# Kernel optimization log

Hardware: AMD Instinct MI355X
Metric: run time of the kernel (lower is better)

The kernel has to match this reference:

```python
import jax, jax.numpy as jnp
import numpy as np

E = 8        # num_experts
TOPK = 2     # num_experts_per_tok
D = 1024     # n_embd
H = 2816     # grok FFN hidden dim (multiple_of-rounded 2/3*4*D)
B, T = 4, 2048
COEFF = 0.01 # moe_aux_loss_coeff


def setup_inputs() -> dict:
    key = jax.random.key(0)
    ks = jax.random.split(key, 8)
    s = 0.02  # weight scale so activations stay well-conditioned
    return {
        "x": jax.random.normal(ks[0], (B, T, D), jnp.float32),
        "gate_w": jax.random.normal(ks[1], (D, E), jnp.float32) * s,
        "expert_gate": jax.random.normal(ks[2], (E, D, H), jnp.float32) * s,
        "expert_up": jax.random.normal(ks[3], (E, D, H), jnp.float32) * s,
        "expert_down": jax.random.normal(ks[4], (E, H, D), jnp.float32) * s,
        "shared_gate": jax.random.normal(ks[5], (D, H), jnp.float32) * s,
        "shared_up": jax.random.normal(ks[6], (D, H), jnp.float32) * s,
        "shared_down": jax.random.normal(ks[7], (H, D), jnp.float32) * s,
    }


def _grok_ffn(x, g, u, d):
    # down(gelu(gate(x)) * up(x)); torch F.gelu default = exact erf gelu
    return (jax.nn.gelu(x @ g, approximate=False) * (x @ u)) @ d


def reference(x, gate_w, expert_gate, expert_up, expert_down,
              shared_gate, shared_up, shared_down):
    Bb, Tt, Dd = x.shape
    N = Bb * Tt
    xf = x.reshape(N, Dd)

    # --- router ---
    logits = (xf @ gate_w).astype(jnp.float32)            # (N, E)
    top_logits, top_idx = jax.lax.top_k(logits, TOPK)     # (N, K)
    top_w = jax.nn.softmax(top_logits, axis=-1)           # (N, K)
    gates = jax.nn.softmax(logits, axis=-1)               # (N, E)
    f = jnp.mean(jax.nn.one_hot(top_idx[:, 0], E, dtype=jnp.float32), axis=0)
    P = gates.mean(axis=0)
    aux_loss = COEFF * E * jnp.sum(f * P)

    # dense combine weights (N, E): 0 for unassigned experts
    comb = jnp.zeros((N, E), xf.dtype).at[
        jnp.arange(N)[:, None], top_idx].add(top_w.astype(xf.dtype))

    # --- experts: loop over small fixed E, weight-masked dense FFN ---
    out = jnp.zeros_like(xf)
    for e in range(E):
        ye = _grok_ffn(xf, expert_gate[e], expert_up[e], expert_down[e])
        out = out + comb[:, e:e + 1] * ye

    out = out.reshape(Bb, Tt, Dd)
    out = out + _grok_ffn(xf, shared_gate, shared_up, shared_down).reshape(Bb, Tt, Dd)
    return out, aux_loss
```

## Files before the change

kernel.cpp:

```cpp
#include <hip/hip_runtime.h>
#include <hip/hip_bf16.h>

#define NTOK 8192
#define DIM  1024
#define HID  2816
#define ROWS_CAP 25600
#define TCAP 200

typedef __bf16 bf16x8 __attribute__((ext_vector_type(8)));
typedef float  f32x4  __attribute__((ext_vector_type(4)));

__device__ __forceinline__ unsigned short f2bf(float f) {
  unsigned int x = __float_as_uint(f);
  unsigned int r = (x + 0x7fffu + ((x >> 16) & 1u)) >> 16;
  return (unsigned short)r;
}
__device__ __forceinline__ float gelu_erf(float g) {
  return 0.5f * g * (1.0f + erff(g * 0.70710678118654752f));
}

__device__ __forceinline__ void gload16(const void* g, void* l) {
  __builtin_amdgcn_global_load_lds(
      (__attribute__((address_space(1))) void*)(g),
      (__attribute__((address_space(3))) void*)(l), 16, 0, 0);
}


__global__ __launch_bounds__(256) void k_transpose_DH(
    const float* __restrict__ eg, const float* __restrict__ eu,
    const float* __restrict__ sg, const float* __restrict__ su,
    unsigned short* __restrict__ WgT, unsigned short* __restrict__ WuT,
    unsigned short* __restrict__ SgT, unsigned short* __restrict__ SuT) {
  __shared__ float t[32][33];
  int z = blockIdx.z;
  const float* in; unsigned short* out;
  if (z < 8)        { in = eg + (size_t)z * DIM * HID;       out = WgT + (size_t)z * DIM * HID; }
  else if (z < 16)  { in = eu + (size_t)(z - 8) * DIM * HID; out = WuT + (size_t)(z - 8) * DIM * HID; }
  else if (z == 16) { in = sg; out = SgT; }
  else              { in = su; out = SuT; }
  const int R = DIM, C = HID;
  int c0 = blockIdx.x * 32, r0 = blockIdx.y * 32;
  int tx = threadIdx.x, ty = threadIdx.y;
  #pragma unroll
  for (int i = ty; i < 32; i += 8)
    t[i][tx] = in[(size_t)(r0 + i) * C + c0 + tx];
  __syncthreads();
  #pragma unroll
  for (int i = ty; i < 32; i += 8)
    out[(size_t)(c0 + i) * R + r0 + tx] = f2bf(t[tx][i]);
}

__global__ __launch_bounds__(256) void k_transpose_HD(
    const float* __restrict__ ed, const float* __restrict__ sd,
    unsigned short* __restrict__ WdT, unsigned short* __restrict__ SdT) {
  __shared__ float t[32][33];
  int z = blockIdx.z;
  const float* in; unsigned short* out;
  if (z < 8) { in = ed + (size_t)z * HID * DIM; out = WdT + (size_t)z * HID * DIM; }
  else       { in = sd; out = SdT; }
  const int R = HID, C = DIM;
  int c0 = blockIdx.x * 32, r0 = blockIdx.y * 32;
  int tx = threadIdx.x, ty = threadIdx.y;
  #pragma unroll
  for (int i = ty; i < 32; i += 8)
    t[i][tx] = in[(size_t)(r0 + i) * C + c0 + tx];
  __syncthreads();
  #pragma unroll
  for (int i = ty; i < 32; i += 8)
    out[(size_t)(c0 + i) * R + r0 + tx] = f2bf(t[tx][i]);
}


__global__ __launch_bounds__(256) void k_router(const float* __restrict__ x,
                                                const float* __restrict__ gw,
                                                unsigned short* __restrict__ xb,
                                                int* __restrict__ top_idx,
                                                float* __restrict__ top_w,
                                                int* __restrict__ counts,
                                                float* __restrict__ f_cnt,
                                                float* __restrict__ P_sum) {
  __shared__ float s_p[8];
  __shared__ int   s_cnt[8];
  __shared__ int   s_f[8];
  int tid = threadIdx.x;
  if (tid < 8) { s_p[tid] = 0.f; s_cnt[tid] = 0; s_f[tid] = 0; }
  __syncthreads();

  int lane = tid & 63, wv = tid >> 6;
  float ploc[8] = {0,0,0,0,0,0,0,0};
  int   cloc[8] = {0,0,0,0,0,0,0,0};
  int   floc[8] = {0,0,0,0,0,0,0,0};

  for (int t = blockIdx.x * 4 + wv; t < NTOK; t += 1024) {
    const float4* xr = (const float4*)(x + (size_t)t * DIM) + lane * 4;
    float4 v0 = xr[0], v1 = xr[1], v2 = xr[2], v3 = xr[3];
    float xv[16] = {v0.x, v0.y, v0.z, v0.w, v1.x, v1.y, v1.z, v1.w,
                    v2.x, v2.y, v2.z, v2.w, v3.x, v3.y, v3.z, v3.w};
    ushort4* xw = (ushort4*)(xb + (size_t)t * DIM + lane * 16);
    #pragma unroll
    for (int q = 0; q < 4; ++q)
      xw[q] = make_ushort4(f2bf(xv[q * 4]), f2bf(xv[q * 4 + 1]),
                           f2bf(xv[q * 4 + 2]), f2bf(xv[q * 4 + 3]));
    float acc[8] = {0.f,0.f,0.f,0.f,0.f,0.f,0.f,0.f};
    #pragma unroll
    for (int i = 0; i < 16; ++i) {
      const float* g = gw + (size_t)(lane * 16 + i) * 8;
      #pragma unroll
      for (int e = 0; e < 8; ++e) acc[e] += xv[i] * g[e];
    }
    #pragma unroll
    for (int e = 0; e < 8; ++e) {
      #pragma unroll
      for (int off = 32; off > 0; off >>= 1)
        acc[e] += __shfl_xor(acc[e], off, 64);
    }
    if (lane == 0) {
      int i1 = 0; float l1 = acc[0];
      #pragma unroll
      for (int e = 1; e < 8; ++e) if (acc[e] > l1) { l1 = acc[e]; i1 = e; }
      int i2 = -1; float l2 = -3.0e38f;
      #pragma unroll
      for (int e = 0; e < 8; ++e) if (e != i1 && acc[e] > l2) { l2 = acc[e]; i2 = e; }
      float e2 = expf(l2 - l1);
      float inv12 = 1.0f / (1.0f + e2);
      top_idx[2 * t] = i1; top_idx[2 * t + 1] = i2;
      top_w[2 * t] = inv12; top_w[2 * t + 1] = e2 * inv12;
      float s = 0.f, p[8];
      #pragma unroll
      for (int e = 0; e < 8; ++e) { p[e] = expf(acc[e] - l1); s += p[e]; }
      float invs = 1.0f / s;
      #pragma unroll
      for (int e = 0; e < 8; ++e) {
        ploc[e] += p[e] * invs;
        cloc[e] += (e == i1) + (e == i2);
        floc[e] += (e == i1);
      }
    }
  }
  if (lane == 0) {
    #pragma unroll
    for (int e = 0; e < 8; ++e) {
      atomicAdd(&s_p[e], ploc[e]);
      atomicAdd(&s_cnt[e], cloc[e]);
      atomicAdd(&s_f[e], floc[e]);
    }
  }
  __syncthreads();
  if (tid < 8) {
    atomicAdd(&P_sum[tid], s_p[tid]);
    atomicAdd(&counts[tid], s_cnt[tid]);
    atomicAdd(&f_cnt[tid], (float)s_f[tid]);
  }
}


__global__ __launch_bounds__(256) void k_setup(const int* __restrict__ counts,
                                               int* __restrict__ cursors,
                                               int* __restrict__ tile_expert,
                                               int* __restrict__ tile_row0,
                                               int* __restrict__ perm,
                                               float* __restrict__ wrow) {
  int t = threadIdx.x;
  for (int r = t; r < ROWS_CAP; r += 256) {
    perm[r] = (r < NTOK) ? r : 0;
    wrow[r] = (r < NTOK) ? 1.0f : 0.0f;
  }
  if (t == 0) {
    int so[8], pe[8];
    int cur = NTOK;
    for (int e = 0; e < 8; ++e) {
      so[e] = cur;
      pe[e] = ((counts[e] + 127) >> 7) << 7;
      cur += pe[e];
    }
    for (int e = 0; e < 8; ++e) cursors[e] = so[e];
    for (int tile = 0; tile < TCAP; ++tile) {
      int r0 = tile << 7;
      int ex;
      if (tile < NTOK / 128) ex = 8;
      else if (r0 < cur) {
        ex = 0;
        for (int e = 0; e < 8; ++e) if (r0 >= so[e] && r0 < so[e] + pe[e]) ex = e;
      } else ex = -1;
      tile_expert[tile] = ex;
      tile_row0[tile] = r0;
    }
  }
}

__global__ __launch_bounds__(256) void k_scatter(const int* __restrict__ top_idx,
                                                 const float* __restrict__ top_w,
                                                 int* __restrict__ cursors,
                                                 int* __restrict__ perm,
                                                 float* __restrict__ wrow) {
  int i = blockIdx.x * 256 + threadIdx.x;
  if (i < NTOK * 2) {
    int e = top_idx[i];
    float w = top_w[i];
    int slot = atomicAdd(&cursors[e], 1);
    perm[slot] = i >> 1;
    wrow[slot] = w;
  }
}


__global__ __launch_bounds__(256) void k_stageA(const unsigned short* __restrict__ xb,
    const unsigned short* __restrict__ WgT, const unsigned short* __restrict__ WuT,
    const unsigned short* __restrict__ SgT, const unsigned short* __restrict__ SuT,
    const int* __restrict__ perm,
    const int* __restrict__ tile_expert, const int* __restrict__ tile_row0,
    unsigned short* __restrict__ h, int t0, int row_base) {
  int tile = t0 + blockIdx.y;
  int e = tile_expert[tile];
  if (e < 0) return;
  const unsigned short* Bg = (e < 8) ? WgT + (size_t)e * HID * DIM : SgT;
  const unsigned short* Bu = (e < 8) ? WuT + (size_t)e * HID * DIM : SuT;
  int rows0 = tile_row0[tile];
  int h0 = blockIdx.x * 64;

  __shared__ unsigned short As[128 * 64];
  __shared__ unsigned short Bgs[64 * 64];
  __shared__ unsigned short Bus[64 * 64];

  int tid = threadIdx.x, lane = tid & 63, wv = tid >> 6;
  int wr = wv >> 1, wc = wv & 1;
  int rlo = lane >> 3;
  int koff = (((lane & 7) ^ rlo) * 8);
  int rsw = (lane & 7) << 4;

  int prow[4];
  #pragma unroll
  for (int i = 0; i < 4; ++i) prow[i] = perm[rows0 + i * 32 + wv * 8 + rlo];
  int bn[2];
  #pragma unroll
  for (int i = 0; i < 2; ++i) bn[i] = h0 + i * 32 + wv * 8 + rlo;

  f32x4 accg[4][2] = {};
  f32x4 accu[4][2] = {};

  for (int kb = 0; kb < DIM / 64; ++kb) {
    int k0 = kb * 64;
    #pragma unroll
    for (int i = 0; i < 4; ++i)
      gload16(xb + (size_t)prow[i] * DIM + k0 + koff, (char*)As + (i * 32 + wv * 8) * 128);
    #pragma unroll
    for (int i = 0; i < 2; ++i) {
      gload16(Bg + (size_t)bn[i] * DIM + k0 + koff, (char*)Bgs + (i * 32 + wv * 8) * 128);
      gload16(Bu + (size_t)bn[i] * DIM + k0 + koff, (char*)Bus + (i * 32 + wv * 8) * 128);
    }
    __syncthreads();
    #pragma unroll
    for (int kk = 0; kk < 2; ++kk) {
      int kbyte = (kk * 64 + (lane >> 4) * 16) ^ rsw;
      bf16x8 a[4], bg[2], bu[2];
      #pragma unroll
      for (int mi = 0; mi < 4; ++mi)
        a[mi] = *(const bf16x8*)((const char*)As + (wr * 64 + mi * 16 + (lane & 15)) * 128 + kbyte);
      #pragma unroll
      for (int ni = 0; ni < 2; ++ni) {
        bg[ni] = *(const bf16x8*)((const char*)Bgs + (wc * 32 + ni * 16 + (lane & 15)) * 128 + kbyte);
        bu[ni] = *(const bf16x8*)((const char*)Bus + (wc * 32 + ni * 16 + (lane & 15)) * 128 + kbyte);
      }
      #pragma unroll
      for (int mi = 0; mi < 4; ++mi) {
        #pragma unroll
        for (int ni = 0; ni < 2; ++ni) {
          accg[mi][ni] = __builtin_amdgcn_mfma_f32_16x16x32_bf16(a[mi], bg[ni], accg[mi][ni], 0, 0, 0);
          accu[mi][ni] = __builtin_amdgcn_mfma_f32_16x16x32_bf16(a[mi], bu[ni], accu[mi][ni], 0, 0, 0);
        }
      }
    }
    __syncthreads();
  }
  #pragma unroll
  for (int mi = 0; mi < 4; ++mi) {
    #pragma unroll
    for (int ni = 0; ni < 2; ++ni) {
      #pragma unroll
      for (int j = 0; j < 4; ++j) {
        int rg = rows0 - row_base + wr * 64 + mi * 16 + (lane >> 4) * 4 + j;
        int cg = h0 + wc * 32 + ni * 16 + (lane & 15);
        float g = accg[mi][ni][j];
        float u = accu[mi][ni][j];
        h[(size_t)rg * HID + cg] = f2bf(gelu_erf(g) * u);
      }
    }
  }
}


template <bool STORE>
__global__ __launch_bounds__(256) void k_stageB(const unsigned short* __restrict__ h,
    const unsigned short* __restrict__ WdT, const unsigned short* __restrict__ SdT,
    const int* __restrict__ perm, const float* __restrict__ wrow,
    const int* __restrict__ tile_expert, const int* __restrict__ tile_row0,
    float* __restrict__ out, int t0, int row_base) {
  int tile = t0 + blockIdx.y;
  int e = tile_expert[tile];
  if (e < 0) return;
  const unsigned short* Bd = (e < 8) ? WdT + (size_t)e * DIM * HID : SdT;
  int rows0 = tile_row0[tile];
  int n0 = blockIdx.x * 128;

  __shared__ unsigned short As[128 * 64];
  __shared__ unsigned short Bs[128 * 64];

  int tid = threadIdx.x, lane = tid & 63, wv = tid >> 6;
  int wr = wv >> 1, wc = wv & 1;
  int rlo = lane >> 3;
  int koff = (((lane & 7) ^ rlo) * 8);
  int rsw = (lane & 7) << 4;

  f32x4 acc[4][4] = {};

  for (int kb = 0; kb < HID / 64; ++kb) {
    int k0 = kb * 64;
    #pragma unroll
    for (int i = 0; i < 4; ++i) {
      int rb = i * 32 + wv * 8;
      int r = rb + rlo;
      gload16(h + (size_t)(rows0 - row_base + r) * HID + k0 + koff, (char*)As + rb * 128);
      gload16(Bd + (size_t)(n0 + r) * HID + k0 + koff, (char*)Bs + rb * 128);
    }
    __syncthreads();
    #pragma unroll
    for (int kk = 0; kk < 2; ++kk) {
      int kbyte = (kk * 64 + (lane >> 4) * 16) ^ rsw;
      bf16x8 a[4], b[4];
      #pragma unroll
      for (int mi = 0; mi < 4; ++mi)
        a[mi] = *(const bf16x8*)((const char*)As + (wr * 64 + mi * 16 + (lane & 15)) * 128 + kbyte);
      #pragma unroll
      for (int ni = 0; ni < 4; ++ni)
        b[ni] = *(const bf16x8*)((const char*)Bs + (wc * 64 + ni * 16 + (lane & 15)) * 128 + kbyte);
      #pragma unroll
      for (int mi = 0; mi < 4; ++mi) {
        #pragma unroll
        for (int ni = 0; ni < 4; ++ni)
          acc[mi][ni] = __builtin_amdgcn_mfma_f32_16x16x32_bf16(a[mi], b[ni], acc[mi][ni], 0, 0, 0);
      }
    }
    __syncthreads();
  }
  #pragma unroll
  for (int mi = 0; mi < 4; ++mi) {
    #pragma unroll
    for (int j = 0; j < 4; ++j) {
      int rl = wr * 64 + mi * 16 + (lane >> 4) * 4 + j;
      int token = perm[rows0 + rl];
      float w = wrow[rows0 + rl];
      #pragma unroll
      for (int ni = 0; ni < 4; ++ni) {
        int col = n0 + wc * 64 + ni * 16 + (lane & 15);
        if (STORE) out[(size_t)token * DIM + col] = w * acc[mi][ni][j];
        else atomicAdd(&out[(size_t)token * DIM + col], w * acc[mi][ni][j]);
      }
    }
  }
}


__global__ void k_aux(const float* __restrict__ f_cnt, const float* __restrict__ P_sum,
                      float* __restrict__ aux_out) {
  if (threadIdx.x == 0 && blockIdx.x == 0) {
    float a = 0.f;
    #pragma unroll
    for (int e = 0; e < 8; ++e) a += f_cnt[e] * P_sum[e];
    a *= 0.01f * 8.f / ((float)NTOK * (float)NTOK);
    aux_out[0] = a;
  }
}


extern "C" void kernel_launch(void* const* d_in, const int* in_sizes, int n_in,
                              void* d_out, int out_size, void* d_ws, size_t ws_size,
                              hipStream_t stream) {
  const float* x  = (const float*)d_in[0];
  const float* gw = (const float*)d_in[1];
  const float* eg = (const float*)d_in[2];
  const float* eu = (const float*)d_in[3];
  const float* ed = (const float*)d_in[4];
  const float* sg = (const float*)d_in[5];
  const float* su = (const float*)d_in[6];
  const float* sd = (const float*)d_in[7];
  float* out = (float*)d_out;

  char* ws = (char*)d_ws;
  size_t off = 0;
  auto take = [&](size_t sz) { size_t o = off; off += (sz + 255) & ~(size_t)255; return o; };
  const size_t OFF_XB   = take((size_t)NTOK * DIM * 2);
  const size_t OFF_WGT  = take((size_t)8 * HID * DIM * 2);
  const size_t OFF_WUT  = take((size_t)8 * HID * DIM * 2);
  const size_t OFF_WDT  = take((size_t)8 * HID * DIM * 2);
  const size_t OFF_SGT  = take((size_t)HID * DIM * 2);
  const size_t OFF_SUT  = take((size_t)HID * DIM * 2);
  const size_t OFF_SDT  = take((size_t)HID * DIM * 2);
  const size_t OFF_TI   = take((size_t)NTOK * 2 * 4);
  const size_t OFF_TW   = take((size_t)NTOK * 2 * 4);
  const size_t OFF_PERM = take((size_t)ROWS_CAP * 4);
  const size_t OFF_WROW = take((size_t)ROWS_CAP * 4);
  const size_t OFF_STATS= take(256);
  const size_t OFF_CURS = take(256);
  const size_t OFF_TE   = take(TCAP * 4);
  const size_t OFF_TR   = take(TCAP * 4);
  const size_t OFF_H    = off;

  const size_t TILE_H_BYTES = (size_t)128 * HID * 2;
  size_t avail = (ws_size > OFF_H) ? (ws_size - OFF_H) : 0;
  int G = (int)((avail / TILE_H_BYTES < (size_t)TCAP) ? (avail / TILE_H_BYTES) : (size_t)TCAP);
  if (G < 1) return;

  unsigned short* xb  = (unsigned short*)(ws + OFF_XB);
  unsigned short* WgT = (unsigned short*)(ws + OFF_WGT);
  unsigned short* WuT = (unsigned short*)(ws + OFF_WUT);
  unsigned short* WdT = (unsigned short*)(ws + OFF_WDT);
  unsigned short* SgT = (unsigned short*)(ws + OFF_SGT);
  unsigned short* SuT = (unsigned short*)(ws + OFF_SUT);
  unsigned short* SdT = (unsigned short*)(ws + OFF_SDT);
  int* top_idx        = (int*)(ws + OFF_TI);
  float* top_w        = (float*)(ws + OFF_TW);
  int* perm           = (int*)(ws + OFF_PERM);
  float* wrow         = (float*)(ws + OFF_WROW);
  int* counts         = (int*)(ws + OFF_STATS);
  float* f_cnt        = (float*)(ws + OFF_STATS + 32);
  float* P_sum        = (float*)(ws + OFF_STATS + 64);
  int* cursors        = (int*)(ws + OFF_CURS);
  int* tile_expert    = (int*)(ws + OFF_TE);
  int* tile_row0      = (int*)(ws + OFF_TR);
  unsigned short* hbuf = (unsigned short*)(ws + OFF_H);

  hipMemsetAsync(ws + OFF_STATS, 0, 256, stream);

  k_transpose_DH<<<dim3(HID / 32, DIM / 32, 18), dim3(32, 8), 0, stream>>>(
      eg, eu, sg, su, WgT, WuT, SgT, SuT);
  k_transpose_HD<<<dim3(DIM / 32, HID / 32, 9), dim3(32, 8), 0, stream>>>(
      ed, sd, WdT, SdT);

  k_router<<<256, 256, 0, stream>>>(x, gw, xb, top_idx, top_w, counts, f_cnt, P_sum);
  k_setup<<<1, 256, 0, stream>>>(counts, cursors, tile_expert, tile_row0, perm, wrow);
  k_scatter<<<NTOK * 2 / 256, 256, 0, stream>>>(top_idx, top_w, cursors, perm, wrow);

  for (int t0 = 0; t0 < TCAP; t0 += G) {
    int nt = (TCAP - t0 < G) ? (TCAP - t0) : G;
    int row_base = t0 * 128;
    k_stageA<<<dim3(HID / 64, nt), 256, 0, stream>>>(xb, WgT, WuT, SgT, SuT, perm,
                                                     tile_expert, tile_row0, hbuf, t0, row_base);
    int ns = 0;
    if (t0 < 64) { ns = 64 - t0; if (ns > nt) ns = nt; }
    int ne = nt - ns;
    if (ns > 0)
      k_stageB<true><<<dim3(DIM / 128, ns), 256, 0, stream>>>(hbuf, WdT, SdT, perm, wrow,
                                                              tile_expert, tile_row0, out, t0, row_base);
    if (ne > 0)
      k_stageB<false><<<dim3(DIM / 128, ne), 256, 0, stream>>>(hbuf, WdT, SdT, perm, wrow,
                                                               tile_expert, tile_row0, out, t0 + ns, row_base);
  }

  k_aux<<<1, 64, 0, stream>>>(f_cnt, P_sum, out + (size_t)NTOK * DIM);
}
```

Before: 977.1 us.

## Double-buffer LDS tiles in both expert GEMM stages to overlap loads with MFMA

Both the gate/up GEMM and the down-projection GEMM now use two LDS buffers. The next K-slice is prefetched through global_load_lds while MFMAs run on the current slice, with explicit vmcnt waits, s_barrier and raised wave priority during compute. The goal is to hide global-memory latency that the previous load-sync-compute-sync loop exposed. LDS use per block doubles, which may lower occupancy, and the hand-coded vmcnt counts must exactly match the number of outstanding loads per stage.

```diff
diff --git a/kernel.cpp b/kernel.cpp
--- a/kernel.cpp
+++ b/kernel.cpp
@@ -218,9 +218,9 @@
   int rows0 = tile_row0[tile];
   int h0 = blockIdx.x * 64;
 
-  __shared__ unsigned short As[128 * 64];
-  __shared__ unsigned short Bgs[64 * 64];
-  __shared__ unsigned short Bus[64 * 64];
+  __shared__ unsigned short As[2][128 * 64];
+  __shared__ unsigned short Bgs[2][64 * 64];
+  __shared__ unsigned short Bus[2][64 * 64];
 
   int tid = threadIdx.x, lane = tid & 63, wv = tid >> 6;
   int wr = wv >> 1, wc = wv & 1;
@@ -238,28 +238,29 @@
   f32x4 accg[4][2] = {};
   f32x4 accu[4][2] = {};
 
-  for (int kb = 0; kb < DIM / 64; ++kb) {
-    int k0 = kb * 64;
+  auto stage = [&](int b, int k0) {
     #pragma unroll
     for (int i = 0; i < 4; ++i)
-      gload16(xb + (size_t)prow[i] * DIM + k0 + koff, (char*)As + (i * 32 + wv * 8) * 128);
+      gload16(xb + (size_t)prow[i] * DIM + k0 + koff, (char*)As[b] + (i * 32 + wv * 8) * 128);
     #pragma unroll
     for (int i = 0; i < 2; ++i) {
-      gload16(Bg + (size_t)bn[i] * DIM + k0 + koff, (char*)Bgs + (i * 32 + wv * 8) * 128);
-      gload16(Bu + (size_t)bn[i] * DIM + k0 + koff, (char*)Bus + (i * 32 + wv * 8) * 128);
-    }
-    __syncthreads();
+      gload16(Bg + (size_t)bn[i] * DIM + k0 + koff, (char*)Bgs[b] + (i * 32 + wv * 8) * 128);
+      gload16(Bu + (size_t)bn[i] * DIM + k0 + koff, (char*)Bus[b] + (i * 32 + wv * 8) * 128);
+    }
+  };
+
+  auto compute = [&](int b) {
     #pragma unroll
     for (int kk = 0; kk < 2; ++kk) {
       int kbyte = (kk * 64 + (lane >> 4) * 16) ^ rsw;
       bf16x8 a[4], bg[2], bu[2];
       #pragma unroll
       for (int mi = 0; mi < 4; ++mi)
-        a[mi] = *(const bf16x8*)((const char*)As + (wr * 64 + mi * 16 + (lane & 15)) * 128 + kbyte);
+        a[mi] = *(const bf16x8*)((const char*)As[b] + (wr * 64 + mi * 16 + (lane & 15)) * 128 + kbyte);
       #pragma unroll
       for (int ni = 0; ni < 2; ++ni) {
-        bg[ni] = *(const bf16x8*)((const char*)Bgs + (wc * 32 + ni * 16 + (lane & 15)) * 128 + kbyte);
-        bu[ni] = *(const bf16x8*)((const char*)Bus + (wc * 32 + ni * 16 + (lane & 15)) * 128 + kbyte);
+        bg[ni] = *(const bf16x8*)((const char*)Bgs[b] + (wc * 32 + ni * 16 + (lane & 15)) * 128 + kbyte);
+        bu[ni] = *(const bf16x8*)((const char*)Bus[b] + (wc * 32 + ni * 16 + (lane & 15)) * 128 + kbyte);
       }
       #pragma unroll
       for (int mi = 0; mi < 4; ++mi) {
@@ -270,8 +271,27 @@
         }
       }
     }
-    __syncthreads();
-  }
+  };
+
+  stage(0, 0);
+  int cur = 0;
+  for (int kb = 0; kb < DIM / 64 - 1; ++kb) {
+    stage(cur ^ 1, (kb + 1) * 64);
+    __builtin_amdgcn_sched_barrier(0);
+    asm volatile("s_waitcnt vmcnt(6)" ::: "memory");
+    __builtin_amdgcn_s_barrier();
+    __builtin_amdgcn_sched_barrier(0);
+    __builtin_amdgcn_s_setprio(1);
+    compute(cur);
+    __builtin_amdgcn_s_setprio(0);
+    __builtin_amdgcn_s_barrier();
+    cur ^= 1;
+  }
+  asm volatile("s_waitcnt vmcnt(0)" ::: "memory");
+  __builtin_amdgcn_s_barrier();
+  __builtin_amdgcn_sched_barrier(0);
+  compute(cur);
+
   #pragma unroll
   for (int mi = 0; mi < 4; ++mi) {
     #pragma unroll
@@ -302,8 +322,8 @@
   int rows0 = tile_row0[tile];
   int n0 = blockIdx.x * 128;
 
-  __shared__ unsigned short As[128 * 64];
-  __shared__ unsigned short Bs[128 * 64];
+  __shared__ unsigned short As[2][128 * 64];
+  __shared__ unsigned short Bs[2][128 * 64];
 
   int tid = threadIdx.x, lane = tid & 63, wv = tid >> 6;
   int wr = wv >> 1, wc = wv & 1;
@@ -313,35 +333,55 @@
 
   f32x4 acc[4][4] = {};
 
-  for (int kb = 0; kb < HID / 64; ++kb) {
-    int k0 = kb * 64;
+  auto stage = [&](int b, int k0) {
     #pragma unroll
     for (int i = 0; i < 4; ++i) {
       int rb = i * 32 + wv * 8;
       int r = rb + rlo;
-      gload16(h + (size_t)(rows0 - row_base + r) * HID + k0 + koff, (char*)As + rb * 128);
-      gload16(Bd + (size_t)(n0 + r) * HID + k0 + koff, (char*)Bs + rb * 128);
-    }
-    __syncthreads();
+      gload16(h + (size_t)(rows0 - row_base + r) * HID + k0 + koff, (char*)As[b] + rb * 128);
+      gload16(Bd + (size_t)(n0 + r) * HID + k0 + koff, (char*)Bs[b] + rb * 128);
+    }
+  };
+
+  auto compute = [&](int b) {
     #pragma unroll
     for (int kk = 0; kk < 2; ++kk) {
       int kbyte = (kk * 64 + (lane >> 4) * 16) ^ rsw;
-      bf16x8 a[4], b[4];
+      bf16x8 a[4], bb[4];
       #pragma unroll
       for (int mi = 0; mi < 4; ++mi)
-        a[mi] = *(const bf16x8*)((const char*)As + (wr * 64 + mi * 16 + (lane & 15)) * 128 + kbyte);
+        a[mi] = *(const bf16x8*)((const char*)As[b] + (wr * 64 + mi * 16 + (lane & 15)) * 128 + kbyte);
       #pragma unroll
       for (int ni = 0; ni < 4; ++ni)
-        b[ni] = *(const bf16x8*)((const char*)Bs + (wc * 64 + ni * 16 + (lane & 15)) * 128 + kbyte);
+        bb[ni] = *(const bf16x8*)((const char*)Bs[b] + (wc * 64 + ni * 16 + (lane & 15)) * 128 + kbyte);
       #pragma unroll
       for (int mi = 0; mi < 4; ++mi) {
         #pragma unroll
         for (int ni = 0; ni < 4; ++ni)
-          acc[mi][ni] = __builtin_amdgcn_mfma_f32_16x16x32_bf16(a[mi], b[ni], acc[mi][ni], 0, 0, 0);
+          acc[mi][ni] = __builtin_amdgcn_mfma_f32_16x16x32_bf16(a[mi], bb[ni], acc[mi][ni], 0, 0, 0);
       }
     }
-    __syncthreads();
-  }
+  };
+
+  stage(0, 0);
+  int cur = 0;
+  for (int kb = 0; kb < HID / 64 - 1; ++kb) {
+    stage(cur ^ 1, (kb + 1) * 64);
+    __builtin_amdgcn_sched_barrier(0);
+    asm volatile("s_waitcnt vmcnt(8)" ::: "memory");
+    __builtin_amdgcn_s_barrier();
+    __builtin_amdgcn_sched_barrier(0);
+    __builtin_amdgcn_s_setprio(1);
+    compute(cur);
+    __builtin_amdgcn_s_setprio(0);
+    __builtin_amdgcn_s_barrier();
+    cur ^= 1;
+  }
+  asm volatile("s_waitcnt vmcnt(0)" ::: "memory");
+  __builtin_amdgcn_s_barrier();
+  __builtin_amdgcn_sched_barrier(0);
+  compute(cur);
+
   #pragma unroll
   for (int mi = 0; mi < 4; ++mi) {
     #pragma unroll
```

Measured after the change: 966.4 us. About the same (-1.1%).
